# Performance work log

Measured on AMD Instinct MI355X. Metric: run time of the kernel, lower is better.

The kernel has to match this reference:

```python
import jax, jax.numpy as jnp
import numpy as np

IN_CH, OUT_CH, K, STRIDE, PAD = 256, 256, 3, 1, 1

# Straight-through-estimator sign (torch Binarize: sign fwd, identity bwd)
@jax.custom_vjp
def ste_sign(x):
    return jnp.sign(x)

def _ste_fwd(x):
    return jnp.sign(x), None

def _ste_bwd(_, g):
    return (g,)

ste_sign.defvjp(_ste_fwd, _ste_bwd)


def setup_inputs() -> dict:
    key = jax.random.key(0)
    ks = jax.random.split(key, 4)
    x = jax.random.normal(ks[0], (32, IN_CH, 56, 56), jnp.float32)
    shift1 = jnp.zeros((1, IN_CH, 1, 1), jnp.float32)
    shift2 = jnp.zeros((1, IN_CH, 1, 1), jnp.float32)
    fan_in = IN_CH * K * K
    weight = jax.random.normal(ks[1], (OUT_CH, IN_CH, K, K), jnp.float32) / np.sqrt(fan_in)
    bias = jax.random.normal(ks[2], (OUT_CH,), jnp.float32) * 0.01
    w1 = jax.random.uniform(ks[3], (1,), jnp.float32) * 0.001  # channel_w scalar
    return {"x": x, "shift1": shift1, "shift2": shift2,
            "weight": weight, "bias": bias, "w1": w1}


def _binarize_conv2d(x, weight, bias):
    # BinarizeConv2d: binarize input (in_ch != 3) and weight via sign, fp conv, add bias
    xb = ste_sign(x)
    wb = ste_sign(weight)
    out = jax.lax.conv_general_dilated(
        xb, wb,
        window_strides=(STRIDE, STRIDE),
        padding=[(PAD, PAD), (PAD, PAD)],
        dimension_numbers=("NCHW", "OIHW", "NCHW"))
    return out + bias[None, :, None, None]


def reference(x, shift1, shift2, weight, bias, w1):
    out1 = _binarize_conv2d(x + shift1, weight, bias)
    out2 = _binarize_conv2d(x + shift2, weight, bias)
    return out1 + w1 * out2
```

## Files before the change

kernel.cpp:

```cpp
#include <hip/hip_runtime.h>
#include <stdint.h>

typedef __attribute__((ext_vector_type(4))) int   i32x4v;
typedef __attribute__((ext_vector_type(16))) int  i32x16v;
typedef __attribute__((ext_vector_type(4))) float f32x4;

#define PIX 3136
#define WW 56
#define SPL 53824
#define SLAB 215296
#define APL 5184
#define ABASE 16384
#define EPQ (32*69*4)
#define LDSB 37120

#define XBP_BYTES ((size_t)32*4*215296)
#define OFF_XBP2  (XBP_BYTES)
#define OFF_WBT   (2*XBP_BYTES)
#define WBT_BYTES ((size_t)9*16*256*16)
#define OFF_FLAG  (OFF_WBT + WBT_BYTES)
#define WS_NEED   (OFF_FLAG + 64)

__global__ __launch_bounds__(256) void k_prep(
    const float* __restrict__ s1, const float* __restrict__ s2,
    const float* __restrict__ w, char* __restrict__ ws,
    char* __restrict__ wbTt, int* __restrict__ flag) {
    int b = blockIdx.x;
    int t = threadIdx.x;
    if (b == 0) {
        __shared__ int bad;
        if (t == 0) bad = 0;
        __syncthreads();
        if (s1[t] != s2[t]) atomicAdd(&bad, 1);
        __syncthreads();
        if (t == 0) *flag = (bad == 0) ? 1 : 0;
        return;
    }
    if (b <= 256) {
        char* base = ws + (size_t)(b - 1) * SLAB;
        int4 z = {0, 0, 0, 0};
#pragma unroll
        for (int i = 0; i < 4; ++i) {
            int u = t + i * 256;
            if (u >= 912) break;
            int s = u / 228, v = u - s * 228;
            int off;
            if (v < 58)       off = v;
            else if (v < 116) off = 3306 + (v - 58);
            else { int r = v - 116; off = ((r >> 1) + 1) * 58 + (r & 1) * 57; }
            *(int4*)(base + s * SPL + off * 16) = z;
        }
        return;
    }
    int idx = (b - 257) * 256 + t;
    int kk = idx >> 16;
    int sub = (idx >> 12) & 15;
    int oc = (idx >> 4) & 255;
    int lo = idx & 15;
    float v = w[(oc * 256 + sub * 16 + lo) * 9 + kk];
    wbTt[idx] = (v > 0.f) ? (char)1 : ((v < 0.f) ? (char)-1 : (char)0);
}

__global__ __launch_bounds__(256) void k_repack_x(
    const float* __restrict__ x, const float* __restrict__ sh1,
    const float* __restrict__ sh2, char* __restrict__ xbp1,
    char* __restrict__ xbp2, const int* __restrict__ flag) {
    __shared__ float lds[64 * 68];
    bool eq = (*flag != 0);
    int t = threadIdx.x;
    int b = blockIdx.x;
    int n = b / 49;
    int p0 = (b % 49) * 64;

    int pixw = t >> 2;
    int sub  = t & 3;
    int pw = p0 + pixw;
    int yw = pw / WW, xw = pw % WW;

    int cl = t >> 4;
    int p4 = (t & 15) * 4;

    for (int cc = 0; cc < 256; cc += 64) {
        __syncthreads();
#pragma unroll
        for (int i = 0; i < 4; ++i) {
            float4 v = *(const float4*)(x + (size_t)(n * 256 + cc + cl + i * 16) * PIX + p0 + p4);
            *(float4*)(&lds[(cl + i * 16) * 68 + p4]) = v;
        }
        __syncthreads();
        size_t obase = (size_t)(n * 4 + (cc >> 6)) * SLAB + (size_t)sub * SPL
                     + ((size_t)(yw + 1) * 58 + (xw + 1)) * 16;
        union { char c[16]; int4 v; } u1, u2;
#pragma unroll
        for (int k = 0; k < 16; ++k) {
            int c = sub * 16 + k;
            float v = lds[c * 68 + pixw];
            float a1 = v + sh1[cc + c];
            float a2 = v + sh2[cc + c];
            u1.c[k] = (a1 > 0.f) ? (char)1 : ((a1 < 0.f) ? (char)-1 : (char)0);
            u2.c[k] = (a2 > 0.f) ? (char)1 : ((a2 < 0.f) ? (char)-1 : (char)0);
        }
        *(int4*)(xbp1 + obase) = u1.v;
        if (!eq) *(int4*)(xbp2 + obase) = u2.v;
    }
}

template <int MODE>
__global__ __launch_bounds__(256, 4) void k_bgemm(
    const char* __restrict__ xsrc, const char* __restrict__ wbTt,
    const float* __restrict__ bias, const float* __restrict__ w1,
    const int* __restrict__ flag, float* __restrict__ out) {
    bool eq = (*flag != 0);
    if (MODE == 0 ? !eq : eq) return;

    __shared__ char lds[LDSB];

    const int t = threadIdx.x;
    const int l = t & 63, wid = t >> 6;
    const int wc = wid & 1;
    const int r32 = l & 31, half = l >> 5;
    const int l16 = l * 16;

    const int logical = (blockIdx.x & 7) * 200 + (blockIdx.x >> 3);
    const int ntile = logical & 1;
    const int m = logical >> 1;
    const int n = m / 25, tp = m % 25;
    const int p0 = tp * 128;
    const int y0 = p0 / WW;
    const int y0c = (y0 < 53) ? y0 : 53;
    const int pxb = p0 + (wid >> 1) * 64;

    int wpm[2];
#pragma unroll
    for (int mi = 0; mi < 2; ++mi) {
        int g = pxb + mi * 32 + r32;
        if (g > 3135) g = 3135;
        int yg = g / WW, xg = g - yg * WW;
        wpm[mi] = (yg + 1 - y0c) * 58 + xg + 1;
    }

    auto stageB = [&](int par, int t2) {
        const int cc2 = t2 / 9, kk2 = t2 % 9;
        const char* src = wbTt
            + ((size_t)((kk2 * 16 + cc2 * 4 + wid) * 256 + ntile * 128)) * 16 + l16;
        char* dst = lds + par * 8192 + wid * 2048;
#pragma unroll
        for (int j = 0; j < 2; ++j)
            __builtin_amdgcn_global_load_lds(
                (const __attribute__((address_space(1))) void*)(src + j * 1024),
                (__attribute__((address_space(3))) void*)(dst + j * 1024), 16, 0, 0);
    };
    auto stageA = [&](int cc2) {
        const char* src = xsrc + (size_t)(n * 4 + cc2) * SLAB + (size_t)wid * SPL
                        + y0c * 928 + l16;
        char* dst = lds + ABASE + wid * APL;
#pragma unroll
        for (int j = 0; j < 5; ++j)
            __builtin_amdgcn_global_load_lds(
                (const __attribute__((address_space(1))) void*)(src + j * 1024),
                (__attribute__((address_space(3))) void*)(dst + j * 1024), 16, 0, 0);
    };

    i32x16v acc[2][2];
#pragma unroll
    for (int mi = 0; mi < 2; ++mi)
#pragma unroll
        for (int nj = 0; nj < 2; ++nj)
#pragma unroll
            for (int i = 0; i < 16; ++i) acc[mi][nj][i] = 0;

    stageA(0);
    stageB(0, 0);
    __syncthreads();

#pragma unroll
    for (int cc = 0; cc < 4; ++cc) {
#pragma unroll
        for (int kk = 0; kk < 9; ++kk) {
            const int tix = cc * 9 + kk;
            if (tix < 35) stageB((tix + 1) & 1, tix + 1);
            const int ts = (kk / 3 - 1) * 58 + (kk % 3) - 1;
            const char* Ab = lds + ABASE;
            const char* Bb = lds + (tix & 1) * 8192;
#pragma unroll
            for (int kq = 0; kq < 2; ++kq) {
                const int ci = kq * 2 + half;
                i32x4v af0 = *(const i32x4v*)(Ab + ci * APL + (wpm[0] + ts) * 16);
                i32x4v af1 = *(const i32x4v*)(Ab + ci * APL + (wpm[1] + ts) * 16);
                i32x4v bf0 = *(const i32x4v*)(Bb + ci * 2048 + (wc * 64 + r32) * 16);
                i32x4v bf1 = *(const i32x4v*)(Bb + ci * 2048 + (wc * 64 + 32 + r32) * 16);
                acc[0][0] = __builtin_amdgcn_mfma_i32_32x32x32_i8(af0, bf0, acc[0][0], 0, 0, 0);
                acc[0][1] = __builtin_amdgcn_mfma_i32_32x32x32_i8(af0, bf1, acc[0][1], 0, 0, 0);
                acc[1][0] = __builtin_amdgcn_mfma_i32_32x32x32_i8(af1, bf0, acc[1][0], 0, 0, 0);
                acc[1][1] = __builtin_amdgcn_mfma_i32_32x32x32_i8(af1, bf1, acc[1][1], 0, 0, 0);
            }
            __syncthreads();
        }
        if (cc < 3) {
            stageA(cc + 1);
            __syncthreads();
        }
    }

    const int ocb = ntile * 128 + wc * 64;
    const bool pvalid = pxb < PIX;
    float w1v = w1[0];
    float se = 1.f + w1v;
    float* sb = (float*)(lds + wid * EPQ);
    size_t outb = (size_t)n * 256 * PIX + pxb;

#pragma unroll
    for (int nj = 0; nj < 2; ++nj) {
        float bv = bias[ocb + nj * 32 + r32];
#pragma unroll
        for (int mi = 0; mi < 2; ++mi)
#pragma unroll
            for (int q = 0; q < 4; ++q) {
                f32x4 v;
#pragma unroll
                for (int j = 0; j < 4; ++j) {
                    float a = (float)(acc[mi][nj][q * 4 + j]);
                    if (MODE == 0)      v[j] = (a + bv) * se;
                    else if (MODE == 1) v[j] = a + se * bv;
                    else                v[j] = w1v * a;
                }
                *(f32x4*)(sb + r32 * 69 + mi * 32 + q * 8 + half * 4) = v;
            }
        asm volatile("s_waitcnt lgkmcnt(0)" ::: "memory");
        if (pvalid) {
#pragma unroll
            for (int p = 0; p < 8; ++p) {
                int row = p * 4 + (l >> 4);
                int px4 = (l & 15) * 4;
                f32x4 v = *(const f32x4*)(sb + row * 69 + px4);
                float* op = out + outb + (size_t)(ocb + nj * 32 + row) * PIX + px4;
                if (MODE == 2) {
                    f32x4 o = *(const f32x4*)op;
                    v[0] += o[0]; v[1] += o[1]; v[2] += o[2]; v[3] += o[3];
                }
                __builtin_nontemporal_store(v, (f32x4*)op);
            }
        }
        if (nj == 0) asm volatile("s_waitcnt lgkmcnt(0)" ::: "memory");
    }
}

extern "C" void kernel_launch(void* const* d_in, const int* in_sizes, int n_in,
                              void* d_out, int out_size, void* d_ws, size_t ws_size,
                              hipStream_t stream) {
    const float* x    = (const float*)d_in[0];
    const float* sh1  = (const float*)d_in[1];
    const float* sh2  = (const float*)d_in[2];
    const float* wgt  = (const float*)d_in[3];
    const float* bias = (const float*)d_in[4];
    const float* w1   = (const float*)d_in[5];
    float* out = (float*)d_out;
    char* ws = (char*)d_ws;
    if (ws_size < WS_NEED) return;

    char* xbp1 = ws;
    char* xbp2 = ws + OFF_XBP2;
    char* wbTt = ws + OFF_WBT;
    int* flag  = (int*)(ws + OFF_FLAG);

    k_prep<<<2561, 256, 0, stream>>>(sh1, sh2, wgt, ws, wbTt, flag);
    k_repack_x<<<32 * 49, 256, 0, stream>>>(x, sh1, sh2, xbp1, xbp2, flag);
    k_bgemm<0><<<1600, 256, 0, stream>>>(xbp1, wbTt, bias, w1, flag, out);
    k_bgemm<1><<<1600, 256, 0, stream>>>(xbp1, wbTt, bias, w1, flag, out);
    k_bgemm<2><<<1600, 256, 0, stream>>>(xbp2, wbTt, bias, w1, flag, out);
}
```

Before: 103.2 us.

## Triple-buffer weight tiles, double-buffer input slabs with fine-grained vmcnt waits

```diff
diff --git a/kernel.cpp b/kernel.cpp
--- a/kernel.cpp
+++ b/kernel.cpp
@@ -10,9 +10,10 @@
 #define SPL 53824
 #define SLAB 215296
 #define APL 5184
-#define ABASE 16384
+#define ABUFSZ 20736
+#define ABASE 24576
 #define EPQ (32*69*4)
-#define LDSB 37120
+#define LDSB 66048
 
 #define XBP_BYTES ((size_t)32*4*215296)
 #define OFF_XBP2  (XBP_BYTES)
@@ -139,21 +140,21 @@
         wpm[mi] = (yg + 1 - y0c) * 58 + xg + 1;
     }
 
-    auto stageB = [&](int par, int t2) {
+    auto stageB = [&](int t2) {
         const int cc2 = t2 / 9, kk2 = t2 % 9;
         const char* src = wbTt
             + ((size_t)((kk2 * 16 + cc2 * 4 + wid) * 256 + ntile * 128)) * 16 + l16;
-        char* dst = lds + par * 8192 + wid * 2048;
+        char* dst = lds + (t2 % 3) * 8192 + wid * 2048;
 #pragma unroll
         for (int j = 0; j < 2; ++j)
             __builtin_amdgcn_global_load_lds(
                 (const __attribute__((address_space(1))) void*)(src + j * 1024),
                 (__attribute__((address_space(3))) void*)(dst + j * 1024), 16, 0, 0);
     };
-    auto stageA = [&](int cc2) {
+    auto stageA = [&](int par, int cc2) {
         const char* src = xsrc + (size_t)(n * 4 + cc2) * SLAB + (size_t)wid * SPL
                         + y0c * 928 + l16;
-        char* dst = lds + ABASE + wid * APL;
+        char* dst = lds + ABASE + par * ABUFSZ + wid * APL;
 #pragma unroll
         for (int j = 0; j < 5; ++j)
             __builtin_amdgcn_global_load_lds(
@@ -169,19 +170,24 @@
 #pragma unroll
             for (int i = 0; i < 16; ++i) acc[mi][nj][i] = 0;
 
-    stageA(0);
-    stageB(0, 0);
-    __syncthreads();
+    stageA(0, 0);
+    stageB(0);
+    stageB(1);
+    asm volatile("s_waitcnt vmcnt(2)" ::: "memory");
+    __builtin_amdgcn_s_barrier();
+    __builtin_amdgcn_sched_barrier(0);
 
 #pragma unroll
     for (int cc = 0; cc < 4; ++cc) {
 #pragma unroll
         for (int kk = 0; kk < 9; ++kk) {
             const int tix = cc * 9 + kk;
-            if (tix < 35) stageB((tix + 1) & 1, tix + 1);
+            if (tix + 2 <= 35) stageB(tix + 2);
+            if (kk == 4 && cc < 3) stageA((cc + 1) & 1, cc + 1);
             const int ts = (kk / 3 - 1) * 58 + (kk % 3) - 1;
-            const char* Ab = lds + ABASE;
-            const char* Bb = lds + (tix & 1) * 8192;
+            const char* Ab = lds + ABASE + (cc & 1) * ABUFSZ;
+            const char* Bb = lds + (tix % 3) * 8192;
+            __builtin_amdgcn_s_setprio(1);
 #pragma unroll
             for (int kq = 0; kq < 2; ++kq) {
                 const int ci = kq * 2 + half;
@@ -194,14 +200,23 @@
                 acc[1][0] = __builtin_amdgcn_mfma_i32_32x32x32_i8(af1, bf0, acc[1][0], 0, 0, 0);
                 acc[1][1] = __builtin_amdgcn_mfma_i32_32x32x32_i8(af1, bf1, acc[1][1], 0, 0, 0);
             }
-            __syncthreads();
-        }
-        if (cc < 3) {
-            stageA(cc + 1);
-            __syncthreads();
-        }
-    }
-
+            __builtin_amdgcn_s_setprio(0);
+            if (tix < 35) {
+                if (tix == 4 || tix == 5 || tix == 13 || tix == 14 ||
+                    tix == 22 || tix == 23) {
+                    asm volatile("s_waitcnt vmcnt(7)" ::: "memory");
+                } else if (tix == 34) {
+                    asm volatile("s_waitcnt vmcnt(0)" ::: "memory");
+                } else {
+                    asm volatile("s_waitcnt vmcnt(2)" ::: "memory");
+                }
+                __builtin_amdgcn_s_barrier();
+                __builtin_amdgcn_sched_barrier(0);
+            }
+        }
+    }
+
+    __syncthreads();
     const int ocb = ntile * 128 + wc * 64;
     const bool pvalid = pxb < PIX;
     float w1v = w1[0];
```

New measurement: 106.2 us. 1.03x slower.
